# Optimization experiments

Hardware: AMD Instinct MI355X
Metric: run time of the kernel (lower is better)

Reference implementation:

```python
import jax, jax.numpy as jnp
import numpy as np
import math

D_MODEL = 1024
D_STATE = 16
D_CONV = 4
EXPAND = 2
D_INNER = EXPAND * D_MODEL
DT_RANK = math.ceil(D_MODEL / 16)
EPS = 1e-5


def setup_inputs() -> dict:
    key = jax.random.key(0)
    ks = jax.random.split(key, 8)
    B, L = 2, 1024
    s = 0.02
    return {
        "hidden_states": jax.random.normal(ks[0], (B, L, D_MODEL), jnp.float32),
        "norm_weight": jnp.ones((D_MODEL,), jnp.float32),
        "in_proj_w": (jax.random.normal(ks[1], (2 * D_INNER, D_MODEL), jnp.float32) * s),
        "conv_w": (jax.random.normal(ks[2], (D_INNER, D_CONV), jnp.float32) * s),
        "conv_b": jnp.zeros((D_INNER,), jnp.float32),
        "x_proj_w": (jax.random.normal(ks[3], (DT_RANK + 2 * D_STATE, D_INNER), jnp.float32) * s),
        "dt_proj_w": (jax.random.normal(ks[4], (D_INNER, DT_RANK), jnp.float32) * s),
        "dt_proj_b": jax.random.uniform(ks[5], (D_INNER,), jnp.float32, -4.0, -2.0),
        "A_log": jnp.log(jnp.broadcast_to(jnp.arange(1, D_STATE + 1, dtype=jnp.float32), (D_INNER, D_STATE))),
        "D": jnp.ones((D_INNER,), jnp.float32),
        "out_proj_w": (jax.random.normal(ks[6], (D_MODEL, D_INNER), jnp.float32) * s),
    }


def _rmsnorm(x, w):
    # Faithful to source: rms = ||x||_2 / sqrt(d); x / (rms + eps) * w
    norm = jnp.linalg.norm(x, axis=-1, keepdims=True)
    rms = norm * (1.0 / math.sqrt(x.shape[-1]))
    return w * (x / (rms + EPS))


def _mamba(h, in_proj_w, conv_w, conv_b, x_proj_w, dt_proj_w, dt_proj_b, A_log, D, out_proj_w):
    B, L, _ = h.shape
    xz = h @ in_proj_w.T                      # (B,L,2*D_INNER)
    x, z = jnp.split(xz, 2, axis=-1)          # each (B,L,D_INNER)

    # causal depthwise conv1d along L, kernel D_CONV
    xpad = jnp.pad(x, ((0, 0), (D_CONV - 1, 0), (0, 0)))
    xc = conv_b
    for k in range(D_CONV):                   # tiny fixed loop over kernel taps
        xc = xc + xpad[:, k:k + L, :] * conv_w[:, k]
    xc = jax.nn.silu(xc)                      # (B,L,D_INNER)

    x_dbl = xc @ x_proj_w.T                   # (B,L,DT_RANK+2N)
    dt, Bm, Cm = jnp.split(x_dbl, [DT_RANK, DT_RANK + D_STATE], axis=-1)
    dt = jax.nn.softplus(dt @ dt_proj_w.T + dt_proj_b)   # (B,L,D_INNER)

    A = -jnp.exp(A_log)                       # (D_INNER,N)
    deltaA = jnp.exp(dt[..., None] * A)                      # (B,L,D_INNER,N)
    deltaBu = (dt * xc)[..., None] * Bm[:, :, None, :]        # (B,L,D_INNER,N)

    def step(hst, inp):
        dA, dBu, Ct = inp
        hst = dA * hst + dBu                  # (B,D_INNER,N)
        y = jnp.einsum('bdn,bn->bd', hst, Ct)
        return hst, y

    h0 = jnp.zeros((B, D_INNER, D_STATE), xc.dtype)
    _, ys = jax.lax.scan(step, h0, (deltaA.swapaxes(0, 1), deltaBu.swapaxes(0, 1), Cm.swapaxes(0, 1)))
    y = ys.swapaxes(0, 1)                     # (B,L,D_INNER)
    y = y + D * xc
    y = y * jax.nn.silu(z)
    return y @ out_proj_w.T                   # (B,L,D_MODEL)


def reference(hidden_states, norm_weight, in_proj_w, conv_w, conv_b, x_proj_w,
              dt_proj_w, dt_proj_b, A_log, D, out_proj_w):
    residual = hidden_states
    h = _rmsnorm(residual, norm_weight)
    out = _mamba(h, in_proj_w, conv_w, conv_b, x_proj_w, dt_proj_w, dt_proj_b,
                 A_log, D, out_proj_w)
    return out, residual
```

## Files before the change

kernel.cpp:

```cpp
#include <hip/hip_runtime.h>

typedef __bf16 bf16x8 __attribute__((ext_vector_type(8)));
typedef float f32x4 __attribute__((ext_vector_type(4)));

__device__ __forceinline__ float b2f(ushort u) {
    union { unsigned int i; float f; } v;
    v.i = ((unsigned int)u) << 16;
    return v.f;
}
__device__ __forceinline__ ushort f2b(float f) {
    union { float f; unsigned int i; } v;
    v.f = f;
    unsigned int x = v.i;
    unsigned int r = (x + 0x7fffu + ((x >> 16) & 1u)) >> 16;
    return (ushort)r;
}
__device__ __forceinline__ float fexp2(float x) {
#if __has_builtin(__builtin_amdgcn_exp2f)
    return __builtin_amdgcn_exp2f(x);
#else
    return exp2f(x);
#endif
}
__device__ __forceinline__ unsigned int packb2(float ap, float h) {
    return ((unsigned int)f2b(h) << 16) | (unsigned int)f2b(ap);
}
__device__ __forceinline__ void gload16(const ushort* g, ushort* l) {
    __builtin_amdgcn_global_load_lds(
        (const __attribute__((address_space(1))) unsigned int*)g,
        (__attribute__((address_space(3))) unsigned int*)l, 16, 0, 0);
}
__device__ __forceinline__ bf16x8 ldsfrag(const ushort* s, int row, int cq) {
    int p = cq ^ (row & 7);
    return *(const bf16x8*)(s + row * 64 + p * 8);
}

#define D_MODEL 1024
#define D_INNER 2048
#define D_STATE 16
#define DT_RANK 64
#define NTOK    2048
#define LSEQ    1024
#define NCH     64
#define LC      16
#define KSL     16
#define LOG2E   1.44269504088896f

__global__ __launch_bounds__(256) void prep_kernel(
    const float* __restrict__ hs, const float* __restrict__ w,
    ushort* __restrict__ hout, float* __restrict__ resid,
    const float* __restrict__ inproj, const float* __restrict__ outproj,
    const float* __restrict__ xprojw, const float* __restrict__ dtw,
    ushort* __restrict__ wIn, ushort* __restrict__ wOut,
    ushort* __restrict__ xpw, ushort* __restrict__ dtwb,
    float* __restrict__ xdbl)
{
    int blk = blockIdx.x;
    int tid = threadIdx.x;
    if (blk < NTOK) {
        int t = blk;
        float4 r4 = *(const float4*)(hs + (size_t)t * D_MODEL + tid * 4);
        float s = r4.x * r4.x + r4.y * r4.y + r4.z * r4.z + r4.w * r4.w;
        #pragma unroll
        for (int off = 32; off >= 1; off >>= 1) s += __shfl_xor(s, off);
        __shared__ float red[4];
        int lane = tid & 63, wid = tid >> 6;
        if (lane == 0) red[wid] = s;
        __syncthreads();
        float tot = red[0] + red[1] + red[2] + red[3];
        float inv = 1.0f / (sqrtf(tot) * (1.0f / 32.0f) + 1e-5f);
        float4 w4 = *(const float4*)(w + tid * 4);
        ushort4 o;
        o.x = f2b(w4.x * r4.x * inv);
        o.y = f2b(w4.y * r4.y * inv);
        o.z = f2b(w4.z * r4.z * inv);
        o.w = f2b(w4.w * r4.w * inv);
        *(ushort4*)(hout + (size_t)t * D_MODEL + tid * 4) = o;
        *(float4*)(resid + (size_t)t * D_MODEL + tid * 4) = r4;
    } else if (blk < NTOK + 6464) {
        int i = (blk - NTOK) * 256 + tid;
        const float* src; ushort* dst; int off;
        if (i < 1048576)      { src = inproj;  dst = wIn;  off = i; }
        else if (i < 1572864) { src = outproj; dst = wOut; off = i - 1048576; }
        else if (i < 1622016) { src = xprojw;  dst = xpw;  off = i - 1572864; }
        else if (i < 1654784) { src = dtw;     dst = dtwb; off = i - 1622016; }
        else return;
        float4 v = *(const float4*)(src + (size_t)off * 4);
        ushort4 o;
        o.x = f2b(v.x); o.y = f2b(v.y); o.z = f2b(v.z); o.w = f2b(v.w);
        *(ushort4*)(dst + (size_t)off * 4) = o;
    } else {
        int i = (blk - NTOK - 6464) * 256 + tid;
        if (i < 49152)
            *(float4*)(xdbl + (size_t)i * 4) = (float4){0.f, 0.f, 0.f, 0.f};
    }
}

__global__ __launch_bounds__(256) void gemm_xz_kernel(
    const ushort* __restrict__ Ag, const ushort* __restrict__ Wg,
    ushort* __restrict__ xq, ushort* __restrict__ zq, int K)
{
    __shared__ __align__(16) ushort smem[128 * 128];
    ushort* sA = smem;
    ushort* sB = smem + 128 * 64;
    int tid = threadIdx.x;
    int bm = blockIdx.x, bn = blockIdx.y;
    int wid = tid >> 6, lane = tid & 63;
    int wm = (wid >> 1) * 64, wn = (wid & 1) * 64;
    int l16 = lane & 15, q = lane >> 4;

    f32x4 acc[4][4];
    #pragma unroll
    for (int i = 0; i < 4; i++)
        #pragma unroll
        for (int j = 0; j < 4; j++)
            acc[i][j] = (f32x4){0.f, 0.f, 0.f, 0.f};

    const ushort* Abase = Ag + (size_t)bm * 128 * K;
    const ushort* Wbase = Wg + (size_t)bn * 128 * K;

    int segr = lane >> 3, segc = lane & 7;
    size_t goff[4]; int sseg[4];
    #pragma unroll
    for (int t = 0; t < 4; t++) {
        int s = wid * 4 + t;
        int r = s * 8 + segr;
        int gc = segc ^ (r & 7);
        sseg[t] = s * 512;
        goff[t] = (size_t)r * K + gc * 8;
    }

    for (int k0 = 0; k0 < K; k0 += 64) {
        __syncthreads();
        #pragma unroll
        for (int t = 0; t < 4; t++) {
            gload16(Abase + goff[t] + k0, sA + sseg[t]);
            gload16(Wbase + goff[t] + k0, sB + sseg[t]);
        }
        __syncthreads();
        #pragma unroll
        for (int ks = 0; ks < 2; ks++) {
            int cq = ks * 4 + q;
            bf16x8 af[4], bfr[4];
            #pragma unroll
            for (int i = 0; i < 4; i++)
                af[i] = ldsfrag(sA, wm + i * 16 + l16, cq);
            #pragma unroll
            for (int j = 0; j < 4; j++)
                bfr[j] = ldsfrag(sB, wn + j * 16 + l16, cq);
            #pragma unroll
            for (int i = 0; i < 4; i++)
                #pragma unroll
                for (int j = 0; j < 4; j++)
                    acc[i][j] = __builtin_amdgcn_mfma_f32_16x16x32_bf16(af[i], bfr[j], acc[i][j], 0, 0, 0);
        }
    }

    __syncthreads();
    #pragma unroll
    for (int i = 0; i < 4; i++)
        #pragma unroll
        for (int j = 0; j < 4; j++) {
            int col = wn + j * 16 + l16;
            int cchunk = col >> 3, cin = col & 7;
            #pragma unroll
            for (int r = 0; r < 4; r++) {
                int row = wm + i * 16 + q * 4 + r;
                smem[row * 128 + ((cchunk ^ (row & 7)) << 3) + cin] =
                    f2b(acc[i][j][r]);
            }
        }
    __syncthreads();
    ushort* dst = (bn < 16) ? xq : zq;
    int colbase = (bn & 15) * 128;
    size_t rowbase = (size_t)bm * 128;
    #pragma unroll
    for (int it = 0; it < 8; it++) {
        int flat = it * 2048 + tid * 8;
        int row = flat >> 7, cchunk = (flat & 127) >> 3;
        *(uint4*)(dst + (rowbase + row) * D_INNER + colbase + (cchunk << 3)) =
            *(const uint4*)(smem + row * 128 + ((cchunk ^ (row & 7)) << 3));
    }
}

__global__ __launch_bounds__(256) void gemm64_kernel(
    const ushort* __restrict__ Ag, const ushort* __restrict__ Wg,
    float* __restrict__ Cf, int M, int N, int K)
{
    __shared__ __align__(16) ushort smem[64 * 128];
    ushort* sA = smem;
    ushort* sB = smem + 64 * 64;
    float* fs = (float*)smem;
    int tid = threadIdx.x;
    int bm = blockIdx.x, bn = blockIdx.y;
    int wid = tid >> 6, lane = tid & 63;
    int wm = wid * 16;
    int l16 = lane & 15, q = lane >> 4;

    f32x4 acc[4];
    #pragma unroll
    for (int j = 0; j < 4; j++) acc[j] = (f32x4){0.f, 0.f, 0.f, 0.f};

    const ushort* Abase = Ag + (size_t)bm * 64 * K;
    const ushort* Wbase = Wg + (size_t)bn * 64 * K;

    int segr = lane >> 3, segc = lane & 7;
    size_t goff[2]; int sseg[2];
    #pragma unroll
    for (int t = 0; t < 2; t++) {
        int s = wid * 2 + t;
        int r = s * 8 + segr;
        int gc = segc ^ (r & 7);
        sseg[t] = s * 512;
        goff[t] = (size_t)r * K + gc * 8;
    }

    for (int k0 = 0; k0 < K; k0 += 64) {
        __syncthreads();
        #pragma unroll
        for (int t = 0; t < 2; t++) {
            gload16(Abase + goff[t] + k0, sA + sseg[t]);
            gload16(Wbase + goff[t] + k0, sB + sseg[t]);
        }
        __syncthreads();
        #pragma unroll
        for (int ks = 0; ks < 2; ks++) {
            int cq = ks * 4 + q;
            bf16x8 af = ldsfrag(sA, wm + l16, cq);
            bf16x8 bfr[4];
            #pragma unroll
            for (int j = 0; j < 4; j++)
                bfr[j] = ldsfrag(sB, j * 16 + l16, cq);
            #pragma unroll
            for (int j = 0; j < 4; j++)
                acc[j] = __builtin_amdgcn_mfma_f32_16x16x32_bf16(af, bfr[j], acc[j], 0, 0, 0);
        }
    }

    __syncthreads();
    #pragma unroll
    for (int j = 0; j < 4; j++)
        #pragma unroll
        for (int r = 0; r < 4; r++)
            fs[(wm + q * 4 + r) * 64 + j * 16 + l16] = acc[j][r];
    __syncthreads();
    #pragma unroll
    for (int it = 0; it < 4; it++) {
        int flat = it * 1024 + tid * 4;
        int row = flat >> 6, col = flat & 63;
        *(float4*)(Cf + (size_t)(bm * 64 + row) * N + bn * 64 + col) =
            *(const float4*)(fs + row * 64 + col);
    }
}

__global__ __launch_bounds__(256) void conv_silu_kernel(
    const ushort* __restrict__ xq, const float* __restrict__ cw,
    const float* __restrict__ cb, ushort* __restrict__ xcb)
{
    int t = blockIdx.x;
    int d0 = threadIdx.x * 8;
    int l = t & (LSEQ - 1), b = t >> 10;

    ushort v[4][8];
    bool has[4];
    #pragma unroll
    for (int k = 0; k < 4; k++) {
        int ll = l - 3 + k;
        has[k] = (ll >= 0);
        if (has[k])
            *(uint4*)v[k] = *(const uint4*)(xq + (((size_t)(b * LSEQ + ll)) << 11) + d0);
    }
    ushort o[8];
    #pragma unroll
    for (int j = 0; j < 8; j++) {
        float4 w4 = *(const float4*)(cw + (size_t)(d0 + j) * 4);
        float wk[4] = {w4.x, w4.y, w4.z, w4.w};
        float acc = cb[d0 + j];
        #pragma unroll
        for (int k = 0; k < 4; k++)
            if (has[k]) acc += b2f(v[k][j]) * wk[k];
        o[j] = f2b(acc / (1.f + __expf(-acc)));
    }
    *(uint4*)(xcb + (((size_t)t) << 11) + d0) = *(const uint4*)o;
}

__global__ __launch_bounds__(256) void xproj_partial_kernel(
    const ushort* __restrict__ xcb, const ushort* __restrict__ wq,
    float* __restrict__ xdbl)
{
    __shared__ __align__(16) ushort sA[128 * 40];
    __shared__ __align__(16) ushort sB[96 * 40];
    int tid = threadIdx.x;
    int bm = blockIdx.x, sl = blockIdx.y;
    int wid = tid >> 6, lane = tid & 63;
    int wm = wid * 32;
    int l16 = lane & 15, q = lane >> 4;

    f32x4 acc[2][6];
    #pragma unroll
    for (int i = 0; i < 2; i++)
        #pragma unroll
        for (int j = 0; j < 6; j++)
            acc[i][j] = (f32x4){0.f, 0.f, 0.f, 0.f};

    const ushort* Abase = xcb + (size_t)bm * 128 * D_INNER;
    int kbase = sl * (D_INNER / KSL);

    for (int kk = 0; kk < D_INNER / KSL; kk += 32) {
        int k0 = kbase + kk;
        __syncthreads();
        #pragma unroll
        for (int i = tid; i < 512; i += 256) {
            int r = i >> 2, c = (i & 3) << 3;
            *(uint4*)(sA + r * 40 + c) = *(const uint4*)(Abase + (size_t)r * D_INNER + k0 + c);
        }
        for (int i = tid; i < 384; i += 256) {
            int r = i >> 2, c = (i & 3) << 3;
            *(uint4*)(sB + r * 40 + c) = *(const uint4*)(wq + (size_t)r * D_INNER + k0 + c);
        }
        __syncthreads();
        bf16x8 af[2], bfr[6];
        #pragma unroll
        for (int i = 0; i < 2; i++)
            af[i] = *(const bf16x8*)(sA + (wm + i * 16 + l16) * 40 + q * 8);
        #pragma unroll
        for (int j = 0; j < 6; j++)
            bfr[j] = *(const bf16x8*)(sB + (j * 16 + l16) * 40 + q * 8);
        #pragma unroll
        for (int i = 0; i < 2; i++)
            #pragma unroll
            for (int j = 0; j < 6; j++)
                acc[i][j] = __builtin_amdgcn_mfma_f32_16x16x32_bf16(af[i], bfr[j], acc[i][j], 0, 0, 0);
    }

    int row0 = bm * 128 + wm + q * 4;
    #pragma unroll
    for (int i = 0; i < 2; i++)
        #pragma unroll
        for (int j = 0; j < 6; j++)
            #pragma unroll
            for (int r = 0; r < 4; r++)
                atomicAdd(&xdbl[(size_t)(row0 + i * 16 + r) * 96 + j * 16 + l16],
                          acc[i][j][r]);
}

__global__ __launch_bounds__(256) void dt_gemm_kernel(
    const float* __restrict__ xdbl, const ushort* __restrict__ dtwq,
    const float* __restrict__ dtb, ushort* __restrict__ dtout)
{
    __shared__ __align__(16) ushort sA[64 * 72];
    __shared__ __align__(16) ushort sB[64 * 72];
    int tid = threadIdx.x;
    int bm = blockIdx.x, bn = blockIdx.y;
    int wid = tid >> 6, lane = tid & 63;
    int wm = wid * 16;
    int l16 = lane & 15, q = lane >> 4;

    const float* Abase = xdbl + (size_t)bm * 64 * 96;
    const ushort* Bbase = dtwq + (size_t)bn * 64 * DT_RANK;
    #pragma unroll
    for (int i = tid; i < 512; i += 256) {
        int r = i >> 3, c = (i & 7) << 3;
        float4 v0 = *(const float4*)(Abase + (size_t)r * 96 + c);
        float4 v1 = *(const float4*)(Abase + (size_t)r * 96 + c + 4);
        ushort o[8] = {f2b(v0.x), f2b(v0.y), f2b(v0.z), f2b(v0.w),
                       f2b(v1.x), f2b(v1.y), f2b(v1.z), f2b(v1.w)};
        *(uint4*)(sA + r * 72 + c) = *(const uint4*)o;
        *(uint4*)(sB + r * 72 + c) = *(const uint4*)(Bbase + (size_t)r * DT_RANK + c);
    }
    __syncthreads();

    f32x4 acc[4];
    #pragma unroll
    for (int j = 0; j < 4; j++) acc[j] = (f32x4){0.f, 0.f, 0.f, 0.f};

    #pragma unroll
    for (int ks = 0; ks < 2; ks++) {
        bf16x8 af = *(const bf16x8*)(sA + (wm + l16) * 72 + ks * 32 + q * 8);
        bf16x8 bfr[4];
        #pragma unroll
        for (int j = 0; j < 4; j++)
            bfr[j] = *(const bf16x8*)(sB + (j * 16 + l16) * 72 + ks * 32 + q * 8);
        #pragma unroll
        for (int j = 0; j < 4; j++)
            acc[j] = __builtin_amdgcn_mfma_f32_16x16x32_bf16(af, bfr[j], acc[j], 0, 0, 0);
    }

    __syncthreads();
    #pragma unroll
    for (int j = 0; j < 4; j++) {
        float bias = dtb[bn * 64 + j * 16 + l16];
        #pragma unroll
        for (int r = 0; r < 4; r++) {
            float s = acc[j][r] + bias;
            float sp = (s > 20.f) ? s : log1pf(__expf(s));
            sA[(wm + q * 4 + r) * 72 + j * 16 + l16] = f2b(sp);
        }
    }
    __syncthreads();
    int row0 = bm * 64, col0 = bn * 64;
    #pragma unroll
    for (int rep = 0; rep < 2; rep++) {
        int off = rep * 2048 + tid * 8;
        int row = off >> 6, col = off & 63;
        *(uint4*)(dtout + (size_t)(row0 + row) * D_INNER + col0 + col) =
            *(const uint4*)(sA + row * 72 + col);
    }
}

__global__ __launch_bounds__(256) void scan_partA_kernel(
    const ushort* __restrict__ dt, const ushort* __restrict__ xcq,
    const float* __restrict__ xdbl, const float* __restrict__ Alog,
    unsigned int* __restrict__ ch)
{
    __shared__ float sBC[LC][32];
    int bid = blockIdx.x;
    int g = bid & 7;
    int c = (bid >> 3) & (NCH - 1);
    int b = bid >> 9;
    int tid = threadIdx.x;
    int lane = tid & 63, wid = tid >> 6;
    int d = g * 256 + wid * 64 + lane;
    int l0 = c * LC;

    if (tid < LC * 8) {
        int r = tid >> 3, c4 = (tid & 7) * 4;
        *(float4*)&sBC[r][c4] =
            *(const float4*)(xdbl + ((size_t)(b * LSEQ + l0 + r)) * 96 + 64 + c4);
    }
    float A[16];
    #pragma unroll
    for (int k = 0; k < 4; k++)
        *(float4*)&A[k * 4] = *(const float4*)(Alog + d * D_STATE + k * 4);
    #pragma unroll
    for (int n = 0; n < 16; n++) A[n] = -__expf(A[n]) * LOG2E;
    __syncthreads();

    const ushort* dtp = dt  + ((size_t)(b * LSEQ + l0)) * D_INNER + d;
    const ushort* xcp = xcq + ((size_t)(b * LSEQ + l0)) * D_INNER + d;

    float h[16];
    #pragma unroll
    for (int n = 0; n < 16; n++) h[n] = 0.f;
    float S = 0.f;

    for (int l = 0; l < LC; l++) {
        float dtv = b2f(dtp[(size_t)l * D_INNER]);
        float xcv = b2f(xcp[(size_t)l * D_INNER]);
        float t = dtv * xcv;
        S += dtv;
        float Bv[16];
        #pragma unroll
        for (int k = 0; k < 4; k++)
            *(float4*)&Bv[k * 4] = *(const float4*)&sBC[l][k * 4];
        #pragma unroll
        for (int n = 0; n < 16; n++) {
            float a = fexp2(dtv * A[n]);
            h[n] = h[n] * a + t * Bv[n];
        }
    }

    unsigned int* outp = ch + (((size_t)(c * 2 + b)) << 15) + (d << 4);
    #pragma unroll
    for (int n = 0; n < 16; n += 4) {
        uint4 v;
        v.x = packb2(fexp2(A[n] * S),     h[n]);
        v.y = packb2(fexp2(A[n + 1] * S), h[n + 1]);
        v.z = packb2(fexp2(A[n + 2] * S), h[n + 2]);
        v.w = packb2(fexp2(A[n + 3] * S), h[n + 3]);
        *(uint4*)&outp[n] = v;
    }
}

__global__ __launch_bounds__(256) void scan_partB_kernel(
    const unsigned int* __restrict__ ch, ushort* __restrict__ hinit)
{
    int kk = blockIdx.x * 256 + threadIdx.x;
    int b = kk >> 15, dn = kk & 32767;
    float run = 0.f;
    #pragma unroll 8
    for (int c = 0; c < NCH; c++) {
        size_t off = (((size_t)(c * 2 + b)) << 15) + dn;
        unsigned int v = ch[off];
        hinit[off] = f2b(run);
        run = b2f((ushort)(v & 0xffffu)) * run + b2f((ushort)(v >> 16));
    }
}

__global__ __launch_bounds__(256) void scan_partC_kernel(
    const ushort* __restrict__ dt, const ushort* __restrict__ xcq,
    const float* __restrict__ xdbl, const ushort* __restrict__ zq,
    const float* __restrict__ Alog, const float* __restrict__ Dp,
    const ushort* __restrict__ hinit, ushort* __restrict__ yg)
{
    __shared__ float sBC[LC][32];
    int bid = blockIdx.x;
    int g = bid & 7;
    int c = (bid >> 3) & (NCH - 1);
    int b = bid >> 9;
    int tid = threadIdx.x;
    int lane = tid & 63, wid = tid >> 6;
    int d = g * 256 + wid * 64 + lane;
    int l0 = c * LC;

    if (tid < LC * 8) {
        int r = tid >> 3, c4 = (tid & 7) * 4;
        *(float4*)&sBC[r][c4] =
            *(const float4*)(xdbl + ((size_t)(b * LSEQ + l0 + r)) * 96 + 64 + c4);
    }
    float A[16];
    #pragma unroll
    for (int k = 0; k < 4; k++)
        *(float4*)&A[k * 4] = *(const float4*)(Alog + d * D_STATE + k * 4);
    #pragma unroll
    for (int n = 0; n < 16; n++) A[n] = -__expf(A[n]) * LOG2E;
    float Dd = Dp[d];

    const ushort* hp = hinit + (((size_t)(c * 2 + b)) << 15) + (d << 4);
    float h[16];
    #pragma unroll
    for (int n = 0; n < 16; n += 4) {
        ushort4 v = *(const ushort4*)(hp + n);
        h[n] = b2f(v.x); h[n + 1] = b2f(v.y);
        h[n + 2] = b2f(v.z); h[n + 3] = b2f(v.w);
    }
    __syncthreads();

    const ushort* dtp = dt  + ((size_t)(b * LSEQ + l0)) * D_INNER + d;
    const ushort* xcp = xcq + ((size_t)(b * LSEQ + l0)) * D_INNER + d;
    const ushort* zp  = zq  + ((size_t)(b * LSEQ + l0)) * D_INNER + d;
    ushort* yp = yg + ((size_t)(b * LSEQ + l0)) * D_INNER + d;

    for (int l = 0; l < LC; l++) {
        float dtv = b2f(dtp[(size_t)l * D_INNER]);
        float xcv = b2f(xcp[(size_t)l * D_INNER]);
        float zv  = b2f(zp[(size_t)l * D_INNER]);
        float t = dtv * xcv;
        float Bv[16], Cv[16];
        #pragma unroll
        for (int k = 0; k < 4; k++) {
            *(float4*)&Bv[k * 4] = *(const float4*)&sBC[l][k * 4];
            *(float4*)&Cv[k * 4] = *(const float4*)&sBC[l][16 + k * 4];
        }
        float p0 = 0.f, p1 = 0.f, p2 = 0.f, p3 = 0.f;
        #pragma unroll
        for (int n = 0; n < 16; n += 4) {
            float a0 = fexp2(dtv * A[n]);
            float a1 = fexp2(dtv * A[n + 1]);
            float a2 = fexp2(dtv * A[n + 2]);
            float a3 = fexp2(dtv * A[n + 3]);
            h[n]     = h[n] * a0 + t * Bv[n];
            h[n + 1] = h[n + 1] * a1 + t * Bv[n + 1];
            h[n + 2] = h[n + 2] * a2 + t * Bv[n + 2];
            h[n + 3] = h[n + 3] * a3 + t * Bv[n + 3];
            p0 += h[n] * Cv[n];
            p1 += h[n + 1] * Cv[n + 1];
            p2 += h[n + 2] * Cv[n + 2];
            p3 += h[n + 3] * Cv[n + 3];
        }
        float p = (p0 + p1) + (p2 + p3);
        float y = p + Dd * xcv;
        float sz = zv / (1.f + __expf(-zv));
        yp[(size_t)l * D_INNER] = f2b(y * sz);
    }
}

extern "C" void kernel_launch(void* const* d_in, const int* in_sizes, int n_in,
                              void* d_out, int out_size, void* d_ws, size_t ws_size,
                              hipStream_t stream)
{
    const float* hs      = (const float*)d_in[0];
    const float* norm_w  = (const float*)d_in[1];
    const float* inproj  = (const float*)d_in[2];
    const float* convw   = (const float*)d_in[3];
    const float* convb   = (const float*)d_in[4];
    const float* xprojw  = (const float*)d_in[5];
    const float* dtw     = (const float*)d_in[6];
    const float* dtb     = (const float*)d_in[7];
    const float* alog    = (const float*)d_in[8];
    const float* dvec    = (const float*)d_in[9];
    const float* outproj = (const float*)d_in[10];

    float* out_main  = (float*)d_out;
    float* out_resid = (float*)d_out + (size_t)NTOK * D_MODEL;

    char* ws = (char*)d_ws;
    ushort*       xq    = (ushort*)(ws);
    ushort*       zq    = (ushort*)(ws +  8388608);
    ushort*       dtq   = (ushort*)(ws + 16777216);
    ushort*       xcb   = (ushort*)(ws + 25165824);
    unsigned int* ch    = (unsigned int*)(ws + 33554432);
    ushort*       hinit = (ushort*)(ws + 50331648);
    float*        xdbl  = (float*) (ws + 67108864);
    ushort*       wIn   = (ushort*)(ws + 67895296);
    ushort*       wOut  = (ushort*)(ws + 76283904);
    ushort*       h_bf16= (ushort*)(ws + 80478208);
    ushort*       xpw_b = (ushort*)(ws + 84672512);
    ushort*       dtw_b = (ushort*)(ws + 85065728);
    ushort*       yg_bf16=(ushort*)(ws + 85327872);

    prep_kernel<<<NTOK + 6464 + 192, 256, 0, stream>>>(
        hs, norm_w, h_bf16, out_resid,
        inproj, outproj, xprojw, dtw, wIn, wOut, xpw_b, dtw_b, xdbl);

    gemm_xz_kernel<<<dim3(NTOK / 128, (2 * D_INNER) / 128), 256, 0, stream>>>(
        h_bf16, wIn, xq, zq, D_MODEL);

    conv_silu_kernel<<<NTOK, 256, 0, stream>>>(xq, convw, convb, xcb);

    xproj_partial_kernel<<<dim3(NTOK / 128, KSL), 256, 0, stream>>>(
        xcb, xpw_b, xdbl);

    dt_gemm_kernel<<<dim3(NTOK / 64, D_INNER / 64), 256, 0, stream>>>(
        xdbl, dtw_b, dtb, dtq);

    scan_partA_kernel<<<1024, 256, 0, stream>>>(dtq, xcb, xdbl, alog, ch);
    scan_partB_kernel<<<256, 256, 0, stream>>>(ch, hinit);
    scan_partC_kernel<<<1024, 256, 0, stream>>>(dtq, xcb, xdbl, zq,
                                                alog, dvec, hinit, yg_bf16);

    gemm64_kernel<<<dim3(NTOK / 64, D_MODEL / 64), 256, 0, stream>>>(
        yg_bf16, wOut, out_main, NTOK, D_MODEL, D_INNER);
}
```

Baseline: 251.3 us.

## Shrink in_proj GEMM tile to 128x64 and split-K out_proj with atomics

The in_proj GEMM tile narrows from 128x128 to 128x64, which doubles the block count from 512 to 1024 and reduces per-wave accumulators, so the CUs are better occupied. The out_proj GEMM is split along K into two halves that atomically add fp32 results into an output buffer, which doubles its grid from 512 to 1024 blocks. That buffer is now zeroed by extra blocks in the prep kernel. The cost is more global atomic traffic, an extra zeroing pass over the output, and lower arithmetic intensity per tile in the in_proj GEMM.

After: 254.3 us. About the same (+1.2%).

```diff
diff --git a/kernel.cpp b/kernel.cpp
--- a/kernel.cpp
+++ b/kernel.cpp
@@ -53,7 +53,7 @@
     const float* __restrict__ xprojw, const float* __restrict__ dtw,
     ushort* __restrict__ wIn, ushort* __restrict__ wOut,
     ushort* __restrict__ xpw, ushort* __restrict__ dtwb,
-    float* __restrict__ xdbl)
+    float* __restrict__ xdbl, float* __restrict__ outz)
 {
     int blk = blockIdx.x;
     int tid = threadIdx.x;
@@ -89,10 +89,14 @@
         ushort4 o;
         o.x = f2b(v.x); o.y = f2b(v.y); o.z = f2b(v.z); o.w = f2b(v.w);
         *(ushort4*)(dst + (size_t)off * 4) = o;
-    } else {
+    } else if (blk < NTOK + 6464 + 192) {
         int i = (blk - NTOK - 6464) * 256 + tid;
         if (i < 49152)
             *(float4*)(xdbl + (size_t)i * 4) = (float4){0.f, 0.f, 0.f, 0.f};
+    } else {
+        int i = (blk - NTOK - 6464 - 192) * 256 + tid;
+        if (i < 524288)
+            *(float4*)(outz + (size_t)i * 4) = (float4){0.f, 0.f, 0.f, 0.f};
     }
 }
 
@@ -100,56 +104,66 @@
     const ushort* __restrict__ Ag, const ushort* __restrict__ Wg,
     ushort* __restrict__ xq, ushort* __restrict__ zq, int K)
 {
-    __shared__ __align__(16) ushort smem[128 * 128];
+    __shared__ __align__(16) ushort smem[128 * 64 + 64 * 64];
     ushort* sA = smem;
     ushort* sB = smem + 128 * 64;
     int tid = threadIdx.x;
     int bm = blockIdx.x, bn = blockIdx.y;
     int wid = tid >> 6, lane = tid & 63;
-    int wm = (wid >> 1) * 64, wn = (wid & 1) * 64;
+    int wm = wid * 32;
     int l16 = lane & 15, q = lane >> 4;
 
-    f32x4 acc[4][4];
-    #pragma unroll
-    for (int i = 0; i < 4; i++)
+    f32x4 acc[2][4];
+    #pragma unroll
+    for (int i = 0; i < 2; i++)
         #pragma unroll
         for (int j = 0; j < 4; j++)
             acc[i][j] = (f32x4){0.f, 0.f, 0.f, 0.f};
 
     const ushort* Abase = Ag + (size_t)bm * 128 * K;
-    const ushort* Wbase = Wg + (size_t)bn * 128 * K;
+    const ushort* Wbase = Wg + (size_t)bn * 64 * K;
 
     int segr = lane >> 3, segc = lane & 7;
-    size_t goff[4]; int sseg[4];
+    size_t goffA[4]; int ssegA[4];
     #pragma unroll
     for (int t = 0; t < 4; t++) {
         int s = wid * 4 + t;
         int r = s * 8 + segr;
         int gc = segc ^ (r & 7);
-        sseg[t] = s * 512;
-        goff[t] = (size_t)r * K + gc * 8;
+        ssegA[t] = s * 512;
+        goffA[t] = (size_t)r * K + gc * 8;
+    }
+    size_t goffB[2]; int ssegB[2];
+    #pragma unroll
+    for (int t = 0; t < 2; t++) {
+        int s = wid * 2 + t;
+        int r = s * 8 + segr;
+        int gc = segc ^ (r & 7);
+        ssegB[t] = s * 512;
+        goffB[t] = (size_t)r * K + gc * 8;
     }
 
     for (int k0 = 0; k0 < K; k0 += 64) {
         __syncthreads();
         #pragma unroll
-        for (int t = 0; t < 4; t++) {
-            gload16(Abase + goff[t] + k0, sA + sseg[t]);
-            gload16(Wbase + goff[t] + k0, sB + sseg[t]);
-        }
+        for (int t = 0; t < 4; t++)
+            gload16(Abase + goffA[t] + k0, sA + ssegA[t]);
+        #pragma unroll
+        for (int t = 0; t < 2; t++)
+            gload16(Wbase + goffB[t] + k0, sB + ssegB[t]);
         __syncthreads();
         #pragma unroll
         for (int ks = 0; ks < 2; ks++) {
             int cq = ks * 4 + q;
-            bf16x8 af[4], bfr[4];
-            #pragma unroll
-            for (int i = 0; i < 4; i++)
+            bf16x8 af[2], bfr[4];
+            #pragma unroll
+            for (int i = 0; i < 2; i++)
                 af[i] = ldsfrag(sA, wm + i * 16 + l16, cq);
             #pragma unroll
             for (int j = 0; j < 4; j++)
-                bfr[j] = ldsfrag(sB, wn + j * 16 + l16, cq);
-            #pragma unroll
-            for (int i = 0; i < 4; i++)
+                bfr[j] = ldsfrag(sB, j * 16 + l16, cq);
+            #pragma unroll
+            for (int i = 0; i < 2; i++)
                 #pragma unroll
                 for (int j = 0; j < 4; j++)
                     acc[i][j] = __builtin_amdgcn_mfma_f32_16x16x32_bf16(af[i], bfr[j], acc[i][j], 0, 0, 0);
@@ -158,28 +172,28 @@
 
     __syncthreads();
     #pragma unroll
-    for (int i = 0; i < 4; i++)
+    for (int i = 0; i < 2; i++)
         #pragma unroll
         for (int j = 0; j < 4; j++) {
-            int col = wn + j * 16 + l16;
+            int col = j * 16 + l16;
             int cchunk = col >> 3, cin = col & 7;
             #pragma unroll
             for (int r = 0; r < 4; r++) {
                 int row = wm + i * 16 + q * 4 + r;
-                smem[row * 128 + ((cchunk ^ (row & 7)) << 3) + cin] =
+                smem[row * 64 + ((cchunk ^ (row & 7)) << 3) + cin] =
                     f2b(acc[i][j][r]);
             }
         }
     __syncthreads();
-    ushort* dst = (bn < 16) ? xq : zq;
-    int colbase = (bn & 15) * 128;
+    ushort* dst = (bn < 32) ? xq : zq;
+    int colbase = (bn & 31) * 64;
     size_t rowbase = (size_t)bm * 128;
     #pragma unroll
-    for (int it = 0; it < 8; it++) {
+    for (int it = 0; it < 4; it++) {
         int flat = it * 2048 + tid * 8;
-        int row = flat >> 7, cchunk = (flat & 127) >> 3;
+        int row = flat >> 6, cchunk = (flat & 63) >> 3;
         *(uint4*)(dst + (rowbase + row) * D_INNER + colbase + (cchunk << 3)) =
-            *(const uint4*)(smem + row * 128 + ((cchunk ^ (row & 7)) << 3));
+            *(const uint4*)(smem + row * 64 + ((cchunk ^ (row & 7)) << 3));
     }
 }
 
@@ -187,12 +201,10 @@
     const ushort* __restrict__ Ag, const ushort* __restrict__ Wg,
     float* __restrict__ Cf, int M, int N, int K)
 {
-    __shared__ __align__(16) ushort smem[64 * 128];
-    ushort* sA = smem;
-    ushort* sB = smem + 64 * 64;
-    float* fs = (float*)smem;
+    __shared__ __align__(16) ushort sA[64 * 64];
+    __shared__ __align__(16) ushort sB[64 * 64];
     int tid = threadIdx.x;
-    int bm = blockIdx.x, bn = blockIdx.y;
+    int bm = blockIdx.x, bn = blockIdx.y, bz = blockIdx.z;
     int wid = tid >> 6, lane = tid & 63;
     int wm = wid * 16;
     int l16 = lane & 15, q = lane >> 4;
@@ -215,7 +227,8 @@
         goff[t] = (size_t)r * K + gc * 8;
     }
 
-    for (int k0 = 0; k0 < K; k0 += 64) {
+    int kbeg = bz * (K / 2), kend = kbeg + K / 2;
+    for (int k0 = kbeg; k0 < kend; k0 += 64) {
         __syncthreads();
         #pragma unroll
         for (int t = 0; t < 2; t++) {
@@ -237,20 +250,13 @@
         }
     }
 
-    __syncthreads();
+    int row0 = bm * 64 + wm + q * 4;
+    int col0 = bn * 64 + l16;
     #pragma unroll
     for (int j = 0; j < 4; j++)
         #pragma unroll
         for (int r = 0; r < 4; r++)
-            fs[(wm + q * 4 + r) * 64 + j * 16 + l16] = acc[j][r];
-    __syncthreads();
-    #pragma unroll
-    for (int it = 0; it < 4; it++) {
-        int flat = it * 1024 + tid * 4;
-        int row = flat >> 6, col = flat & 63;
-        *(float4*)(Cf + (size_t)(bm * 64 + row) * N + bn * 64 + col) =
-            *(const float4*)(fs + row * 64 + col);
-    }
+            atomicAdd(&Cf[(size_t)(row0 + r) * N + col0 + j * 16], acc[j][r]);
 }
 
 __global__ __launch_bounds__(256) void conv_silu_kernel(
@@ -599,11 +605,11 @@
     ushort*       dtw_b = (ushort*)(ws + 85065728);
     ushort*       yg_bf16=(ushort*)(ws + 85327872);
 
-    prep_kernel<<<NTOK + 6464 + 192, 256, 0, stream>>>(
+    prep_kernel<<<NTOK + 6464 + 192 + 2048, 256, 0, stream>>>(
         hs, norm_w, h_bf16, out_resid,
-        inproj, outproj, xprojw, dtw, wIn, wOut, xpw_b, dtw_b, xdbl);
-
-    gemm_xz_kernel<<<dim3(NTOK / 128, (2 * D_INNER) / 128), 256, 0, stream>>>(
+        inproj, outproj, xprojw, dtw, wIn, wOut, xpw_b, dtw_b, xdbl, out_main);
+
+    gemm_xz_kernel<<<dim3(NTOK / 128, (2 * D_INNER) / 64), 256, 0, stream>>>(
         h_bf16, wIn, xq, zq, D_MODEL);
 
     conv_silu_kernel<<<NTOK, 256, 0, stream>>>(xq, convw, convb, xcb);
@@ -619,6 +625,6 @@
     scan_partC_kernel<<<1024, 256, 0, stream>>>(dtq, xcb, xdbl, zq,
                                                 alog, dvec, hinit, yg_bf16);
 
-    gemm64_kernel<<<dim3(NTOK / 64, D_MODEL / 64), 256, 0, stream>>>(
+    gemm64_kernel<<<dim3(NTOK / 64, D_MODEL / 64, 2), 256, 0, stream>>>(
         yg_bf16, wOut, out_main, NTOK, D_MODEL, D_INNER);
 }
```

## Fuse causal depthwise conv and SiLU into the in-projection GEMM epilogue

Applied to the files above, without the earlier changes.

The x-half of the in-projection GEMM now applies the 4-tap causal conv and SiLU directly from the shared-memory output tile and writes xcb, instead of storing x and running a separate conv kernel. Rows whose taps cross the 128-row tile boundary are handled by a small fixup kernel that reads saved boundary rows. This removes the full write and re-read of the x activation and one kernel launch. In exchange the GEMM epilogue carries extra ALU work and there is an added small launch.

After: 234.3 us. 1.07x faster.

```diff
diff --git a/kernel.cpp b/kernel.cpp
--- a/kernel.cpp
+++ b/kernel.cpp
@@ -98,9 +98,13 @@
 
 __global__ __launch_bounds__(256) void gemm_xz_kernel(
     const ushort* __restrict__ Ag, const ushort* __restrict__ Wg,
-    ushort* __restrict__ xq, ushort* __restrict__ zq, int K)
+    const float* __restrict__ cw, const float* __restrict__ cb,
+    ushort* __restrict__ xcb, ushort* __restrict__ xb,
+    ushort* __restrict__ zq, int K)
 {
     __shared__ __align__(16) ushort smem[128 * 128];
+    __shared__ float cwl[128][4];
+    __shared__ float cbl[128];
     ushort* sA = smem;
     ushort* sB = smem + 128 * 64;
     int tid = threadIdx.x;
@@ -108,6 +112,15 @@
     int wid = tid >> 6, lane = tid & 63;
     int wm = (wid >> 1) * 64, wn = (wid & 1) * 64;
     int l16 = lane & 15, q = lane >> 4;
+    int colbase = (bn & 15) * 128;
+
+    if (bn < 16 && tid < 128) {
+        cwl[tid][0] = cw[(size_t)(colbase + tid) * 4 + 0];
+        cwl[tid][1] = cw[(size_t)(colbase + tid) * 4 + 1];
+        cwl[tid][2] = cw[(size_t)(colbase + tid) * 4 + 2];
+        cwl[tid][3] = cw[(size_t)(colbase + tid) * 4 + 3];
+        cbl[tid] = cb[colbase + tid];
+    }
 
     f32x4 acc[4][4];
     #pragma unroll
@@ -171,16 +184,89 @@
             }
         }
     __syncthreads();
-    ushort* dst = (bn < 16) ? xq : zq;
-    int colbase = (bn & 15) * 128;
     size_t rowbase = (size_t)bm * 128;
-    #pragma unroll
-    for (int it = 0; it < 8; it++) {
-        int flat = it * 2048 + tid * 8;
-        int row = flat >> 7, cchunk = (flat & 127) >> 3;
-        *(uint4*)(dst + (rowbase + row) * D_INNER + colbase + (cchunk << 3)) =
-            *(const uint4*)(smem + row * 128 + ((cchunk ^ (row & 7)) << 3));
-    }
+
+    if (bn >= 16) {
+        int cb2 = (bn - 16) * 128;
+        #pragma unroll
+        for (int it = 0; it < 8; it++) {
+            int flat = it * 2048 + tid * 8;
+            int row = flat >> 7, cchunk = (flat & 127) >> 3;
+            *(uint4*)(zq + (rowbase + row) * D_INNER + cb2 + (cchunk << 3)) =
+                *(const uint4*)(smem + row * 128 + ((cchunk ^ (row & 7)) << 3));
+        }
+        return;
+    }
+
+    if (tid < 96) {
+        int rr = tid >> 4;
+        int row = (rr < 3) ? rr : (125 + rr - 3);
+        int chunk = tid & 15;
+        *(uint4*)(xb + (size_t)(bm * 6 + rr) * D_INNER + colbase + chunk * 8) =
+            *(const uint4*)(smem + row * 128 + ((chunk ^ (row & 7)) << 3));
+    }
+
+    for (int idx = tid; idx < 2000; idx += 256) {
+        int row = (idx >> 4) + 3;
+        int chunk = idx & 15;
+        ushort tap[4][8];
+        #pragma unroll
+        for (int k = 0; k < 4; k++) {
+            int rk = row - 3 + k;
+            *(uint4*)tap[k] =
+                *(const uint4*)(smem + rk * 128 + ((chunk ^ (rk & 7)) << 3));
+        }
+        ushort o[8];
+        #pragma unroll
+        for (int j = 0; j < 8; j++) {
+            int cl = chunk * 8 + j;
+            float acc2 = cbl[cl];
+            #pragma unroll
+            for (int k = 0; k < 4; k++)
+                acc2 += b2f(tap[k][j]) * cwl[cl][k];
+            o[j] = f2b(acc2 / (1.f + __expf(-acc2)));
+        }
+        *(uint4*)(xcb + (rowbase + row) * D_INNER + colbase + chunk * 8) =
+            *(const uint4*)o;
+    }
+}
+
+__global__ __launch_bounds__(256) void conv_fixup_kernel(
+    const ushort* __restrict__ xb, const float* __restrict__ cw,
+    const float* __restrict__ cb, ushort* __restrict__ xcb)
+{
+    int bm = blockIdx.x / 3;
+    int r  = blockIdx.x % 3;
+    int d0 = threadIdx.x * 8;
+
+    ushort tap[4][8];
+    bool has[4];
+    #pragma unroll
+    for (int k = 0; k < 4; k++) {
+        int rt = r - 3 + k;
+        if (rt < 0 && (bm & 7) == 0) {
+            has[k] = false;
+        } else {
+            has[k] = true;
+            int bmm, slot;
+            if (rt < 0) { bmm = bm - 1; slot = rt + 6; }
+            else        { bmm = bm;     slot = rt; }
+            *(uint4*)tap[k] =
+                *(const uint4*)(xb + (size_t)(bmm * 6 + slot) * D_INNER + d0);
+        }
+    }
+    ushort o[8];
+    #pragma unroll
+    for (int j = 0; j < 8; j++) {
+        float4 w4 = *(const float4*)(cw + (size_t)(d0 + j) * 4);
+        float wk[4] = {w4.x, w4.y, w4.z, w4.w};
+        float acc = cb[d0 + j];
+        #pragma unroll
+        for (int k = 0; k < 4; k++)
+            if (has[k]) acc += b2f(tap[k][j]) * wk[k];
+        o[j] = f2b(acc / (1.f + __expf(-acc)));
+    }
+    *(uint4*)(xcb + (size_t)(bm * 128 + r) * D_INNER + d0) = *(const uint4*)o;
 }
 
 __global__ __launch_bounds__(256) void gemm64_kernel(
@@ -251,37 +337,6 @@
         *(float4*)(Cf + (size_t)(bm * 64 + row) * N + bn * 64 + col) =
             *(const float4*)(fs + row * 64 + col);
     }
-}
-
-__global__ __launch_bounds__(256) void conv_silu_kernel(
-    const ushort* __restrict__ xq, const float* __restrict__ cw,
-    const float* __restrict__ cb, ushort* __restrict__ xcb)
-{
-    int t = blockIdx.x;
-    int d0 = threadIdx.x * 8;
-    int l = t & (LSEQ - 1), b = t >> 10;
-
-    ushort v[4][8];
-    bool has[4];
-    #pragma unroll
-    for (int k = 0; k < 4; k++) {
-        int ll = l - 3 + k;
-        has[k] = (ll >= 0);
-        if (has[k])
-            *(uint4*)v[k] = *(const uint4*)(xq + (((size_t)(b * LSEQ + ll)) << 11) + d0);
-    }
-    ushort o[8];
-    #pragma unroll
-    for (int j = 0; j < 8; j++) {
-        float4 w4 = *(const float4*)(cw + (size_t)(d0 + j) * 4);
-        float wk[4] = {w4.x, w4.y, w4.z, w4.w};
-        float acc = cb[d0 + j];
-        #pragma unroll
-        for (int k = 0; k < 4; k++)
-            if (has[k]) acc += b2f(v[k][j]) * wk[k];
-        o[j] = f2b(acc / (1.f + __expf(-acc)));
-    }
-    *(uint4*)(xcb + (((size_t)t) << 11) + d0) = *(const uint4*)o;
 }
 
 __global__ __launch_bounds__(256) void xproj_partial_kernel(
@@ -585,7 +640,7 @@
     float* out_resid = (float*)d_out + (size_t)NTOK * D_MODEL;
 
     char* ws = (char*)d_ws;
-    ushort*       xq    = (ushort*)(ws);
+    ushort*       xb    = (ushort*)(ws);
     ushort*       zq    = (ushort*)(ws +  8388608);
     ushort*       dtq   = (ushort*)(ws + 16777216);
     ushort*       xcb   = (ushort*)(ws + 25165824);
@@ -604,9 +659,9 @@
         inproj, outproj, xprojw, dtw, wIn, wOut, xpw_b, dtw_b, xdbl);
 
     gemm_xz_kernel<<<dim3(NTOK / 128, (2 * D_INNER) / 128), 256, 0, stream>>>(
-        h_bf16, wIn, xq, zq, D_MODEL);
-
-    conv_silu_kernel<<<NTOK, 256, 0, stream>>>(xq, convw, convb, xcb);
+        h_bf16, wIn, convw, convb, xcb, xb, zq, D_MODEL);
+
+    conv_fixup_kernel<<<48, 256, 0, stream>>>(xb, convw, convb, xcb);
 
     xproj_partial_kernel<<<dim3(NTOK / 128, KSL), 256, 0, stream>>>(
         xcb, xpw_b, xdbl);
```
